# Kernel optimization log

Measured on AMD Instinct MI355X. Metric: run time of the kernel, lower is better.

Reference implementation:

```python
import jax, jax.numpy as jnp
import numpy as np

DEPTH, HEADS, DIM, DHEAD, MLP = 4, 16, 1024, 64, 4096
B, N, M = 4, 1024, 1024
EPS = 1e-5


def layer_norm(x, w, b):
    mu = jnp.mean(x, axis=-1, keepdims=True)
    var = jnp.var(x, axis=-1, keepdims=True)
    return (x - mu) * jax.lax.rsqrt(var + EPS) * w + b


def setup_inputs() -> dict:
    key = jax.random.key(0)
    ks = jax.random.split(key, 16)
    inner = HEADS * DHEAD
    s = lambda fan_in: 1.0 / np.sqrt(fan_in)
    # weights stored in (in, out) layout: y = x @ W + b
    return {
        "x": jax.random.normal(ks[0], (B, N, DIM), jnp.float32),
        "m": jax.random.normal(ks[1], (B, M, DIM), jnp.float32),
        "Wq": jax.random.normal(ks[2], (DEPTH, DIM, inner), jnp.float32) * s(DIM),
        "Wk": jax.random.normal(ks[3], (DEPTH, DIM, inner), jnp.float32) * s(DIM),
        "Wv": jax.random.normal(ks[4], (DEPTH, DIM, inner), jnp.float32) * s(DIM),
        "Wo": jax.random.normal(ks[5], (DEPTH, inner, DIM), jnp.float32) * s(inner),
        "bo": jnp.zeros((DEPTH, DIM), jnp.float32),
        "ln1_w": jnp.ones((DEPTH, DIM), jnp.float32),
        "ln1_b": jnp.zeros((DEPTH, DIM), jnp.float32),
        "W1": jax.random.normal(ks[6], (DEPTH, DIM, MLP), jnp.float32) * s(DIM),
        "b1": jnp.zeros((DEPTH, MLP), jnp.float32),
        "W2": jax.random.normal(ks[7], (DEPTH, MLP, DIM), jnp.float32) * s(MLP),
        "b2": jnp.zeros((DEPTH, DIM), jnp.float32),
        "ln2_w": jnp.ones((DEPTH, DIM), jnp.float32),
        "ln2_b": jnp.zeros((DEPTH, DIM), jnp.float32),
    }


def reference(x, m, Wq, Wk, Wv, Wo, bo, ln1_w, ln1_b, W1, b1, W2, b2, ln2_w, ln2_b):
    scale = DIM ** (-0.5)  # NOTE: original scales by dim**-0.5, not dim_head**-0.5
    for i in range(DEPTH):
        # cross-attention block (PreNorm on x only; m is used raw, as in source)
        h = layer_norm(x, ln1_w[i], ln1_b[i])
        q = jnp.einsum('bnd,de->bne', h, Wq[i]).reshape(B, N, HEADS, DHEAD)
        k = jnp.einsum('bmd,de->bme', m, Wk[i]).reshape(B, M, HEADS, DHEAD)
        v = jnp.einsum('bmd,de->bme', m, Wv[i]).reshape(B, M, HEADS, DHEAD)
        dots = jnp.einsum('bihd,bjhd->bhij', q, k) * scale
        attn = jax.nn.softmax(dots, axis=-1)
        out = jnp.einsum('bhij,bjhd->bihd', attn, v).reshape(B, N, HEADS * DHEAD)
        x = x + jnp.einsum('bne,ed->bnd', out, Wo[i]) + bo[i]
        # feed-forward block
        h2 = layer_norm(x, ln2_w[i], ln2_b[i])
        ff = jax.nn.gelu(jnp.einsum('bnd,df->bnf', h2, W1[i]) + b1[i], approximate=False)
        x = x + jnp.einsum('bnf,fd->bnd', ff, W2[i]) + b2[i]
    return x
```

## Files before the change

kernel.cpp:

```cpp
#include <hip/hip_runtime.h>
#include <hip/hip_bf16.h>
#include <math.h>

typedef __hip_bfloat16 bf16;
typedef __attribute__((ext_vector_type(8))) short bf16x8;
typedef __attribute__((ext_vector_type(4))) float f32x4;

#define DEPTH  4
#define HEADS  16
#define DIM    1024
#define DHEAD  64
#define MLPD   4096
#define BB     4
#define NN     1024
#define MMK    1024
#define ROWS   (BB*NN)
#define QKVS   3072

__device__ inline float bitsbf(short s) {
  union { float f; unsigned u; } c; c.u = ((unsigned)(unsigned short)s) << 16; return c.f;
}
__device__ inline short bfbits(float f) {
  bf16 h = __float2bfloat16(f); return *(short*)&h;
}

__device__ inline void gload_lds16(const bf16* g, bf16* l) {
  __builtin_amdgcn_global_load_lds((const __attribute__((address_space(1))) unsigned int*)g,
                                   (__attribute__((address_space(3))) unsigned int*)l, 16, 0, 0);
}

__global__ __launch_bounds__(256) void f2b_kernel(const float* __restrict__ in, bf16* __restrict__ out, int n) {
  int i = blockIdx.x * 256 + threadIdx.x;
  if (i < n) out[i] = __float2bfloat16(in[i]);
}

__global__ __launch_bounds__(256) void transpose_f2b(const float* __restrict__ in, bf16* __restrict__ out,
                                                     int inStride, int rowOff, int colOff, int outStride) {
  __shared__ float tile[32][33];
  int n0 = blockIdx.x * 32, k0 = blockIdx.y * 32;
  int tx = threadIdx.x, ty = threadIdx.y;
  #pragma unroll
  for (int i = 0; i < 32; i += 8)
    tile[ty + i][tx] = in[(size_t)(rowOff + k0 + ty + i) * inStride + colOff + n0 + tx];
  __syncthreads();
  #pragma unroll
  for (int i = 0; i < 32; i += 8)
    out[(size_t)(n0 + ty + i) * outStride + k0 + tx] = __float2bfloat16(tile[tx][ty + i]);
}

__global__ __launch_bounds__(256) void ln_kernel(const float* __restrict__ x, const float* __restrict__ w,
                                                 const float* __restrict__ b, bf16* __restrict__ out) {
  int row = blockIdx.x, t = threadIdx.x;
  const float* xr = x + (size_t)row * DIM;
  float4 xv = *(const float4*)(xr + t * 4);
  float s  = xv.x + xv.y + xv.z + xv.w;
  float s2 = xv.x * xv.x + xv.y * xv.y + xv.z * xv.z + xv.w * xv.w;
  #pragma unroll
  for (int off = 32; off; off >>= 1) { s += __shfl_xor(s, off, 64); s2 += __shfl_xor(s2, off, 64); }
  __shared__ float sh_s[4], sh_s2[4], sh_mu, sh_rstd;
  int wid = t >> 6;
  if ((t & 63) == 0) { sh_s[wid] = s; sh_s2[wid] = s2; }
  __syncthreads();
  if (t == 0) {
    float S1 = sh_s[0] + sh_s[1] + sh_s[2] + sh_s[3];
    float S2 = sh_s2[0] + sh_s2[1] + sh_s2[2] + sh_s2[3];
    float mu = S1 * (1.0f / DIM);
    float var = S2 * (1.0f / DIM) - mu * mu;
    sh_mu = mu; sh_rstd = rsqrtf(var + 1e-5f);
  }
  __syncthreads();
  float mu = sh_mu, rstd = sh_rstd;
  float4 wv = *(const float4*)(w + t * 4);
  float4 bv = *(const float4*)(b + t * 4);
  bf16* orow = out + (size_t)row * DIM + t * 4;
  orow[0] = __float2bfloat16((xv.x - mu) * rstd * wv.x + bv.x);
  orow[1] = __float2bfloat16((xv.y - mu) * rstd * wv.y + bv.y);
  orow[2] = __float2bfloat16((xv.z - mu) * rstd * wv.z + bv.z);
  orow[3] = __float2bfloat16((xv.w - mu) * rstd * wv.w + bv.w);
}

#define MODE_PLAIN 0
#define MODE_GELU  1
#define MODE_RES   2
#define BM 128
#define BK 32

template<int JT>
__global__ __launch_bounds__(256) void gemm_tile(const bf16* __restrict__ A, const bf16* __restrict__ Bt,
                                                 const float* __restrict__ bias, bf16* __restrict__ outb,
                                                 float* __restrict__ resf, int outStride, int K, int mode) {
  constexpr int BN = JT * 32;
  __shared__ __align__(16) bf16 As[2][BM * BK];
  __shared__ __align__(16) bf16 Bs[2][BN * BK];
  int t = threadIdx.x;
  int w = t >> 6, l = t & 63;
  int l15 = l & 15, quad = l >> 4;
  int col0 = blockIdx.x * BN, row0 = blockIdx.y * BM;
  int wm = (w >> 1) * 64, wn = (w & 1) * (JT * 16);

  f32x4 acc[4][JT] = {};

  int sm = w * 16 + (l >> 2);
  int sk = (l & 3) * 8;
  const bf16* ag0 = A  + (size_t)(row0 + sm) * K + sk;
  const bf16* ag1 = A  + (size_t)(row0 + 64 + sm) * K + sk;
  const bf16* bg0 = Bt + (size_t)(col0 + sm) * K + sk;
  const bf16* bg1 = Bt + (size_t)(col0 + 64 + sm) * K + sk;

  gload_lds16(ag0, &As[0][w * 512]);
  gload_lds16(ag1, &As[0][2048 + w * 512]);
  gload_lds16(bg0, &Bs[0][w * 512]);
  if constexpr (JT == 4) gload_lds16(bg1, &Bs[0][2048 + w * 512]);

  int cur = 0;
  for (int k0 = 0; k0 < K; k0 += BK) {
    __syncthreads();
    int nxt = cur ^ 1;
    if (k0 + BK < K) {
      gload_lds16(ag0 + k0 + BK, &As[nxt][w * 512]);
      gload_lds16(ag1 + k0 + BK, &As[nxt][2048 + w * 512]);
      gload_lds16(bg0 + k0 + BK, &Bs[nxt][w * 512]);
      if constexpr (JT == 4) gload_lds16(bg1 + k0 + BK, &Bs[nxt][2048 + w * 512]);
    }
    bf16x8 af[4], bfr[JT];
    #pragma unroll
    for (int i = 0; i < 4; ++i)  af[i]  = *(const bf16x8*)&As[cur][(wm + i * 16 + l15) * BK + quad * 8];
    #pragma unroll
    for (int j = 0; j < JT; ++j) bfr[j] = *(const bf16x8*)&Bs[cur][(wn + j * 16 + l15) * BK + quad * 8];
    #pragma unroll
    for (int i = 0; i < 4; ++i)
      #pragma unroll
      for (int j = 0; j < JT; ++j)
        acc[i][j] = __builtin_amdgcn_mfma_f32_16x16x32_bf16(af[i], bfr[j], acc[i][j], 0, 0, 0);
    cur = nxt;
  }

  #pragma unroll
  for (int i = 0; i < 4; ++i) {
    #pragma unroll
    for (int j = 0; j < JT; ++j) {
      int gcol = col0 + wn + j * 16 + l15;
      float bval = (mode != MODE_PLAIN && bias != nullptr) ? bias[gcol] : 0.0f;
      #pragma unroll
      for (int r = 0; r < 4; ++r) {
        int grow = row0 + wm + i * 16 + quad * 4 + r;
        float val = acc[i][j][r];
        size_t idx = (size_t)grow * outStride + gcol;
        if (mode == MODE_RES) {
          resf[idx] = resf[idx] + val + bval;
        } else {
          if (mode == MODE_GELU) {
            float u = val + bval;
            val = 0.5f * u * (1.0f + erff(u * 0.70710678118654752f));
          }
          outb[idx] = __float2bfloat16(val);
        }
      }
    }
  }
}

#define ALDP 72

__global__ __launch_bounds__(256) void attn_mfma_kernel(const bf16* __restrict__ qkv, bf16* __restrict__ o) {
  __shared__ __align__(16) bf16  Kl[2][64 * 64];
  __shared__ __align__(16) short Vt[2][64][ALDP];
  __shared__ __align__(16) short Pl[64][ALDP];

  int t = threadIdx.x;
  int lane = t & 63, w = t >> 6;
  int l15 = lane & 15, quad = lane >> 4;
  int bh = blockIdx.x;
  int qt = blockIdx.y;
  int b = bh >> 4, hh = bh & 15;

  const bf16* q = qkv;
  const bf16* k = qkv + 1024;
  const bf16* v = qkv + 2048;

  int krow = w * 16 + (lane >> 3);
  int kcol = ((lane & 7) ^ (lane >> 3)) * 8;
  const bf16* kg0 = k + (size_t)(b * MMK + krow) * QKVS + hh * DHEAD + kcol;
  const bf16* kg1 = kg0 + (size_t)8 * QKVS;

  int srow = t >> 2, sc0 = (t & 3) * 16;
  const bf16* vg = v + (size_t)(b * MMK + srow) * QKVS + hh * DHEAD + sc0;

  bf16x8 qfrag[2];
  {
    const bf16* qp = q + (size_t)(b * NN + qt * 64 + w * 16 + l15) * QKVS + hh * DHEAD + quad * 8;
    #pragma unroll
    for (int ks = 0; ks < 2; ++ks) {
      bf16x8 raw = *(const bf16x8*)(qp + ks * 32);
      bf16x8 sc;
      #pragma unroll
      for (int e = 0; e < 8; ++e) sc[e] = bfbits(bitsbf(raw[e]) * 0.03125f);
      qfrag[ks] = sc;
    }
  }

  gload_lds16(kg0, &Kl[0][w * 1024]);
  gload_lds16(kg1, &Kl[0][w * 1024 + 512]);
  {
    bf16x8 v0 = *(const bf16x8*)vg;
    bf16x8 v1 = *(const bf16x8*)(vg + 8);
    #pragma unroll
    for (int e = 0; e < 8; ++e) {
      Vt[0][sc0 + e][srow]     = v0[e];
      Vt[0][sc0 + 8 + e][srow] = v1[e];
    }
  }

  f32x4 Oacc[4] = {{}, {}, {}, {}};
  float mrow[4] = {-1e30f, -1e30f, -1e30f, -1e30f};
  float lrow[4] = {0.f, 0.f, 0.f, 0.f};

  int cur = 0;
  for (int kt = 0; kt < MMK / 64; ++kt) {
    __syncthreads();
    int nxt = cur ^ 1;
    bool more = (kt + 1 < MMK / 64);
    bf16x8 nv0, nv1;
    if (more) {
      const bf16* vgn = vg + (size_t)(kt + 1) * 64 * QKVS;
      nv0 = *(const bf16x8*)vgn;
      nv1 = *(const bf16x8*)(vgn + 8);
      gload_lds16(kg0 + (size_t)(kt + 1) * 64 * QKVS, &Kl[nxt][w * 1024]);
      gload_lds16(kg1 + (size_t)(kt + 1) * 64 * QKVS, &Kl[nxt][w * 1024 + 512]);
    }

    f32x4 S[4] = {{}, {}, {}, {}};
    #pragma unroll
    for (int ks = 0; ks < 2; ++ks) {
      #pragma unroll
      for (int j = 0; j < 4; ++j) {
        bf16x8 bfr = *(const bf16x8*)&Kl[cur][(j * 16 + l15) * 64 + (((ks * 4 + quad) ^ (l15 & 7)) * 8)];
        S[j] = __builtin_amdgcn_mfma_f32_16x16x32_bf16(qfrag[ks], bfr, S[j], 0, 0, 0);
      }
    }

    #pragma unroll
    for (int r = 0; r < 4; ++r) {
      float tm = fmaxf(fmaxf(S[0][r], S[1][r]), fmaxf(S[2][r], S[3][r]));
      tm = fmaxf(tm, __shfl_xor(tm, 1, 64));
      tm = fmaxf(tm, __shfl_xor(tm, 2, 64));
      tm = fmaxf(tm, __shfl_xor(tm, 4, 64));
      tm = fmaxf(tm, __shfl_xor(tm, 8, 64));
      float mn = fmaxf(mrow[r], tm);
      float alpha = __expf(mrow[r] - mn);
      mrow[r] = mn;
      float rs = 0.f;
      #pragma unroll
      for (int j = 0; j < 4; ++j) {
        float p = __expf(S[j][r] - mn);
        S[j][r] = p;
        rs += p;
      }
      rs += __shfl_xor(rs, 1, 64);
      rs += __shfl_xor(rs, 2, 64);
      rs += __shfl_xor(rs, 4, 64);
      rs += __shfl_xor(rs, 8, 64);
      lrow[r] = lrow[r] * alpha + rs;
      #pragma unroll
      for (int j = 0; j < 4; ++j) {
        Oacc[j][r] *= alpha;
        Pl[w * 16 + quad * 4 + r][j * 16 + l15] = bfbits(S[j][r]);
      }
    }

    #pragma unroll
    for (int ks = 0; ks < 2; ++ks) {
      bf16x8 pa = *(const bf16x8*)&Pl[w * 16 + l15][ks * 32 + quad * 8];
      #pragma unroll
      for (int j = 0; j < 4; ++j) {
        bf16x8 vb = *(const bf16x8*)&Vt[cur][j * 16 + l15][ks * 32 + quad * 8];
        Oacc[j] = __builtin_amdgcn_mfma_f32_16x16x32_bf16(pa, vb, Oacc[j], 0, 0, 0);
      }
    }

    if (more) {
      #pragma unroll
      for (int e = 0; e < 8; ++e) {
        Vt[nxt][sc0 + e][srow]     = nv0[e];
        Vt[nxt][sc0 + 8 + e][srow] = nv1[e];
      }
    }
    cur = nxt;
  }

  #pragma unroll
  for (int r = 0; r < 4; ++r) {
    float inv = 1.0f / lrow[r];
    bf16* op = o + (size_t)(b * NN + qt * 64 + w * 16 + quad * 4 + r) * DIM + hh * DHEAD;
    #pragma unroll
    for (int j = 0; j < 4; ++j)
      op[j * 16 + l15] = __float2bfloat16(Oacc[j][r] * inv);
  }
}

extern "C" void kernel_launch(void* const* d_in, const int* in_sizes, int n_in,
                              void* d_out, int out_size, void* d_ws, size_t ws_size,
                              hipStream_t stream) {
  const float* x_in = (const float*)d_in[0];
  const float* m    = (const float*)d_in[1];
  const float* Wq   = (const float*)d_in[2];
  const float* Wk   = (const float*)d_in[3];
  const float* Wv   = (const float*)d_in[4];
  const float* Wo   = (const float*)d_in[5];
  const float* bo   = (const float*)d_in[6];
  const float* ln1w = (const float*)d_in[7];
  const float* ln1b = (const float*)d_in[8];
  const float* W1   = (const float*)d_in[9];
  const float* b1   = (const float*)d_in[10];
  const float* W2   = (const float*)d_in[11];
  const float* b2   = (const float*)d_in[12];
  const float* ln2w = (const float*)d_in[13];
  const float* ln2b = (const float*)d_in[14];

  float* xf = (float*)d_out;

  char* ws = (char*)d_ws;
  bf16* h    = (bf16*)(ws + 0);
  bf16* mb   = (bf16*)(ws + (8u  << 20));
  bf16* qkv  = (bf16*)(ws + (16u << 20));
  bf16* ffh  = (bf16*)(ws + (16u << 20));
  bf16* wt   = (bf16*)(ws + (40u << 20));

  const int NTOK = ROWS * DIM;

  hipMemcpyAsync(xf, x_in, (size_t)NTOK * sizeof(float), hipMemcpyDeviceToDevice, stream);
  f2b_kernel<<<dim3((NTOK + 255) / 256), dim3(256), 0, stream>>>(m, mb, NTOK);

  dim3 blk(256);
  dim3 tblk(32, 8);
  dim3 g_1k(DIM / 128, ROWS / BM);
  dim3 g_2k(2048 / 128, ROWS / BM);
  dim3 tr_1k(DIM / 32, DIM / 32);
  dim3 tr_w1(2048 / 32, DIM / 32);
  dim3 tr_w2(DIM / 32, 2048 / 32);
  dim3 attn_grid(BB * HEADS, NN / 64);

  for (int L = 0; L < DEPTH; ++L) {
    const float* WqL = Wq + (size_t)L * DIM * DIM;
    const float* WkL = Wk + (size_t)L * DIM * DIM;
    const float* WvL = Wv + (size_t)L * DIM * DIM;
    const float* WoL = Wo + (size_t)L * DIM * DIM;
    const float* W1L = W1 + (size_t)L * DIM * MLPD;
    const float* W2L = W2 + (size_t)L * MLPD * DIM;

    ln_kernel<<<dim3(ROWS), blk, 0, stream>>>(xf, ln1w + L * DIM, ln1b + L * DIM, h);

    transpose_f2b<<<tr_1k, tblk, 0, stream>>>(WkL, wt, DIM, 0, 0, DIM);
    transpose_f2b<<<tr_1k, tblk, 0, stream>>>(WvL, wt + 1024 * 1024, DIM, 0, 0, DIM);
    gemm_tile<4><<<g_2k, blk, 0, stream>>>(mb, wt, nullptr, qkv + 1024, nullptr, QKVS, DIM, MODE_PLAIN);

    transpose_f2b<<<tr_1k, tblk, 0, stream>>>(WqL, wt, DIM, 0, 0, DIM);
    gemm_tile<4><<<g_1k, blk, 0, stream>>>(h, wt, nullptr, qkv, nullptr, QKVS, DIM, MODE_PLAIN);

    attn_mfma_kernel<<<attn_grid, blk, 0, stream>>>(qkv, h);

    transpose_f2b<<<tr_1k, tblk, 0, stream>>>(WoL, wt, DIM, 0, 0, DIM);
    gemm_tile<4><<<g_1k, blk, 0, stream>>>(h, wt, bo + L * DIM, nullptr, xf, DIM, DIM, MODE_RES);

    ln_kernel<<<dim3(ROWS), blk, 0, stream>>>(xf, ln2w + L * DIM, ln2b + L * DIM, h);

    for (int half = 0; half < 2; ++half) {
      transpose_f2b<<<tr_w1, tblk, 0, stream>>>(W1L, wt, MLPD, 0, half * 2048, DIM);
      gemm_tile<4><<<g_2k, blk, 0, stream>>>(h, wt, b1 + (size_t)L * MLPD + half * 2048, ffh, nullptr,
                                             2048, DIM, MODE_GELU);
      transpose_f2b<<<tr_w2, tblk, 0, stream>>>(W2L, wt, DIM, half * 2048, 0, 2048);
      gemm_tile<4><<<g_1k, blk, 0, stream>>>(ffh, wt, (half == 0) ? (b2 + (size_t)L * DIM) : nullptr,
                                             nullptr, xf, DIM, 2048, MODE_RES);
    }
  }
}
```

Before: 1.834 ms.

## Double GEMM K-tile to 64 with XOR-swizzled LDS and narrower tiles for N=1024 GEMMs

The GEMM k-step grows from 32 to 64 with two MFMA sub-steps per stage, halving the barrier and loop overhead per unit of work. LDS rows are XOR-swizzled to avoid bank conflicts on the wider rows. GEMMs with 1024 output columns now use JT=2 (64-wide tiles), doubling block count for better CU occupancy. This costs more LDS per block and less B-operand reuse for the narrow tiles.

Result: faster. 1.549 ms (-15.5%).

```diff
diff --git a/kernel.cpp b/kernel.cpp
--- a/kernel.cpp
+++ b/kernel.cpp
@@ -83,55 +83,66 @@
 #define MODE_GELU  1
 #define MODE_RES   2
 #define BM 128
-#define BK 32
+#define BK2 64
 
 template<int JT>
 __global__ __launch_bounds__(256) void gemm_tile(const bf16* __restrict__ A, const bf16* __restrict__ Bt,
                                                  const float* __restrict__ bias, bf16* __restrict__ outb,
                                                  float* __restrict__ resf, int outStride, int K, int mode) {
   constexpr int BN = JT * 32;
-  __shared__ __align__(16) bf16 As[2][BM * BK];
-  __shared__ __align__(16) bf16 Bs[2][BN * BK];
+  __shared__ __align__(16) bf16 As[2][BM * BK2];
+  __shared__ __align__(16) bf16 Bs[2][BN * BK2];
   int t = threadIdx.x;
   int w = t >> 6, l = t & 63;
   int l15 = l & 15, quad = l >> 4;
+  int l8 = l & 7, lh = l >> 3;
   int col0 = blockIdx.x * BN, row0 = blockIdx.y * BM;
   int wm = (w >> 1) * 64, wn = (w & 1) * (JT * 16);
 
   f32x4 acc[4][JT] = {};
 
-  int sm = w * 16 + (l >> 2);
-  int sk = (l & 3) * 8;
-  const bf16* ag0 = A  + (size_t)(row0 + sm) * K + sk;
-  const bf16* ag1 = A  + (size_t)(row0 + 64 + sm) * K + sk;
-  const bf16* bg0 = Bt + (size_t)(col0 + sm) * K + sk;
-  const bf16* bg1 = Bt + (size_t)(col0 + 64 + sm) * K + sk;
-
-  gload_lds16(ag0, &As[0][w * 512]);
-  gload_lds16(ag1, &As[0][2048 + w * 512]);
-  gload_lds16(bg0, &Bs[0][w * 512]);
-  if constexpr (JT == 4) gload_lds16(bg1, &Bs[0][2048 + w * 512]);
+  int swk = (l8 ^ lh) * 8;
+  const bf16* agB = A  + (size_t)(row0 + w * 32 + lh) * K + swk;
+  const bf16* bgB = Bt + (size_t)(col0 + (JT == 4 ? w * 32 : w * 16) + lh) * K + swk;
+
+  #pragma unroll
+  for (int i = 0; i < 4; ++i)
+    gload_lds16(agB + (size_t)(i * 8) * K, &As[0][w * 2048 + i * 512]);
+  #pragma unroll
+  for (int i = 0; i < (JT == 4 ? 4 : 2); ++i)
+    gload_lds16(bgB + (size_t)(i * 8) * K, &Bs[0][w * (JT == 4 ? 2048 : 1024) + i * 512]);
 
   int cur = 0;
-  for (int k0 = 0; k0 < K; k0 += BK) {
+  for (int k0 = 0; k0 < K; k0 += BK2) {
     __syncthreads();
     int nxt = cur ^ 1;
-    if (k0 + BK < K) {
-      gload_lds16(ag0 + k0 + BK, &As[nxt][w * 512]);
-      gload_lds16(ag1 + k0 + BK, &As[nxt][2048 + w * 512]);
-      gload_lds16(bg0 + k0 + BK, &Bs[nxt][w * 512]);
-      if constexpr (JT == 4) gload_lds16(bg1 + k0 + BK, &Bs[nxt][2048 + w * 512]);
-    }
-    bf16x8 af[4], bfr[JT];
-    #pragma unroll
-    for (int i = 0; i < 4; ++i)  af[i]  = *(const bf16x8*)&As[cur][(wm + i * 16 + l15) * BK + quad * 8];
-    #pragma unroll
-    for (int j = 0; j < JT; ++j) bfr[j] = *(const bf16x8*)&Bs[cur][(wn + j * 16 + l15) * BK + quad * 8];
-    #pragma unroll
-    for (int i = 0; i < 4; ++i)
-      #pragma unroll
-      for (int j = 0; j < JT; ++j)
-        acc[i][j] = __builtin_amdgcn_mfma_f32_16x16x32_bf16(af[i], bfr[j], acc[i][j], 0, 0, 0);
+    if (k0 + BK2 < K) {
+      #pragma unroll
+      for (int i = 0; i < 4; ++i)
+        gload_lds16(agB + (size_t)(i * 8) * K + k0 + BK2, &As[nxt][w * 2048 + i * 512]);
+      #pragma unroll
+      for (int i = 0; i < (JT == 4 ? 4 : 2); ++i)
+        gload_lds16(bgB + (size_t)(i * 8) * K + k0 + BK2, &Bs[nxt][w * (JT == 4 ? 2048 : 1024) + i * 512]);
+    }
+    #pragma unroll
+    for (int ks2 = 0; ks2 < 2; ++ks2) {
+      bf16x8 af[4], bfr[JT];
+      #pragma unroll
+      for (int i = 0; i < 4; ++i) {
+        int R = wm + i * 16 + l15;
+        af[i] = *(const bf16x8*)&As[cur][R * 64 + (((quad + 4 * ks2) ^ (l15 & 7)) * 8)];
+      }
+      #pragma unroll
+      for (int j = 0; j < JT; ++j) {
+        int R = wn + j * 16 + l15;
+        bfr[j] = *(const bf16x8*)&Bs[cur][R * 64 + (((quad + 4 * ks2) ^ (l15 & 7)) * 8)];
+      }
+      #pragma unroll
+      for (int i = 0; i < 4; ++i)
+        #pragma unroll
+        for (int j = 0; j < JT; ++j)
+          acc[i][j] = __builtin_amdgcn_mfma_f32_16x16x32_bf16(af[i], bfr[j], acc[i][j], 0, 0, 0);
+    }
     cur = nxt;
   }
 
@@ -333,8 +344,8 @@
 
   dim3 blk(256);
   dim3 tblk(32, 8);
-  dim3 g_1k(DIM / 128, ROWS / BM);
-  dim3 g_2k(2048 / 128, ROWS / BM);
+  dim3 g_n1(DIM / 64, ROWS / BM);
+  dim3 g_n2(2048 / 128, ROWS / BM);
   dim3 tr_1k(DIM / 32, DIM / 32);
   dim3 tr_w1(2048 / 32, DIM / 32);
   dim3 tr_w2(DIM / 32, 2048 / 32);
@@ -352,24 +363,24 @@
 
     transpose_f2b<<<tr_1k, tblk, 0, stream>>>(WkL, wt, DIM, 0, 0, DIM);
     transpose_f2b<<<tr_1k, tblk, 0, stream>>>(WvL, wt + 1024 * 1024, DIM, 0, 0, DIM);
-    gemm_tile<4><<<g_2k, blk, 0, stream>>>(mb, wt, nullptr, qkv + 1024, nullptr, QKVS, DIM, MODE_PLAIN);
+    gemm_tile<4><<<g_n2, blk, 0, stream>>>(mb, wt, nullptr, qkv + 1024, nullptr, QKVS, DIM, MODE_PLAIN);
 
     transpose_f2b<<<tr_1k, tblk, 0, stream>>>(WqL, wt, DIM, 0, 0, DIM);
-    gemm_tile<4><<<g_1k, blk, 0, stream>>>(h, wt, nullptr, qkv, nullptr, QKVS, DIM, MODE_PLAIN);
+    gemm_tile<2><<<g_n1, blk, 0, stream>>>(h, wt, nullptr, qkv, nullptr, QKVS, DIM, MODE_PLAIN);
 
     attn_mfma_kernel<<<attn_grid, blk, 0, stream>>>(qkv, h);
 
     transpose_f2b<<<tr_1k, tblk, 0, stream>>>(WoL, wt, DIM, 0, 0, DIM);
-    gemm_tile<4><<<g_1k, blk, 0, stream>>>(h, wt, bo + L * DIM, nullptr, xf, DIM, DIM, MODE_RES);
+    gemm_tile<2><<<g_n1, blk, 0, stream>>>(h, wt, bo + L * DIM, nullptr, xf, DIM, DIM, MODE_RES);
 
     ln_kernel<<<dim3(ROWS), blk, 0, stream>>>(xf, ln2w + L * DIM, ln2b + L * DIM, h);
 
     for (int half = 0; half < 2; ++half) {
       transpose_f2b<<<tr_w1, tblk, 0, stream>>>(W1L, wt, MLPD, 0, half * 2048, DIM);
-      gemm_tile<4><<<g_2k, blk, 0, stream>>>(h, wt, b1 + (size_t)L * MLPD + half * 2048, ffh, nullptr,
+      gemm_tile<4><<<g_n2, blk, 0, stream>>>(h, wt, b1 + (size_t)L * MLPD + half * 2048, ffh, nullptr,
                                              2048, DIM, MODE_GELU);
       transpose_f2b<<<tr_w2, tblk, 0, stream>>>(W2L, wt, DIM, half * 2048, 0, 2048);
-      gemm_tile<4><<<g_1k, blk, 0, stream>>>(ffh, wt, (half == 0) ? (b2 + (size_t)L * DIM) : nullptr,
+      gemm_tile<2><<<g_n1, blk, 0, stream>>>(ffh, wt, (half == 0) ? (b2 + (size_t)L * DIM) : nullptr,
                                              nullptr, xf, DIM, 2048, MODE_RES);
     }
   }
```
